# Optimization experiments

Measured on AMD Instinct MI355X. Metric: run time of the kernel, lower is better.

The kernel has to match this reference:

```python
import jax, jax.numpy as jnp
import numpy as np

NUM_HEADS = 6

def setup_inputs() -> dict:
    key = jax.random.key(0)
    ks = jax.random.split(key, 5)
    B, N, C = 4096, 49, 192
    nW = 64
    x = jax.random.normal(ks[0], (B, N, C), dtype=jnp.float32)
    mask = jax.random.normal(ks[1], (nW, 1, N, N), dtype=jnp.float32)
    w_qkv = jax.random.normal(ks[2], (C, 3 * C), dtype=jnp.float32) * (C ** -0.5)
    w_proj = jax.random.normal(ks[3], (C, C), dtype=jnp.float32) * (C ** -0.5)
    b_proj = jnp.zeros((C,), dtype=jnp.float32)
    return {"x": x, "mask": mask, "w_qkv": w_qkv, "w_proj": w_proj, "b_proj": b_proj}

def reference(x, mask, w_qkv, w_proj, b_proj):
    B, N, C = x.shape
    H = NUM_HEADS
    d = C // H
    nW = mask.shape[0]
    scale = d ** -0.5
    # fused QKV projection: [B, N, 3, H, d]
    qkv = (x @ w_qkv).reshape(B, N, 3, H, d)
    q = qkv[:, :, 0] * scale          # [B, N, H, d]
    k = qkv[:, :, 1]
    v = qkv[:, :, 2]
    # scaled attention scores per head: [B, H, N, N]
    attn = jnp.einsum('bnhd,bmhd->bhnm', q, k)
    # additive window mask, broadcast over heads
    attn = attn.reshape(B // nW, nW, H, N, N) + mask
    attn = attn.reshape(B, H, N, N)
    attn = jax.nn.softmax(attn, axis=-1)
    # attention-weighted values, back to [B, N, C]
    out = jnp.einsum('bhnm,bmhd->bnhd', attn, v).reshape(B, N, C)
    return out @ w_proj + b_proj
```

## Files before the change

### kernel.cpp

```cpp
#include <hip/hip_runtime.h>

using bf16_t = __bf16;
using bf16x4 = __bf16 __attribute__((ext_vector_type(4)));
using bf16x8 = __bf16 __attribute__((ext_vector_type(8)));
using f32x4  = float  __attribute__((ext_vector_type(4)));

#define MFMA16(a, b, c) __builtin_amdgcn_mfma_f32_16x16x32_bf16((a), (b), (c), 0, 0, 0)

__device__ __forceinline__ bf16x8 ld_b8_2x(const bf16_t* p) {
    bf16x4 lo = *(const bf16x4*)p;
    bf16x4 hi = *(const bf16x4*)(p + 4);
    bf16x8 r;
    r[0] = lo[0]; r[1] = lo[1]; r[2] = lo[2]; r[3] = lo[3];
    r[4] = hi[0]; r[5] = hi[1]; r[6] = hi[2]; r[7] = hi[3];
    return r;
}

__global__ void prep_weights(const float* __restrict__ wqkv,
                             const float* __restrict__ wproj,
                             bf16_t* __restrict__ wA,
                             bf16_t* __restrict__ w2B) {
    int idx = blockIdx.x * 256 + threadIdx.x;
    const int N1 = 36 * 6 * 64 * 8;
    if (idx < N1) {
        int j = idx & 7, L = (idx >> 3) & 63, q = idx >> 9;
        int ks = q % 6, mt = q / 6;
        int cc = ks * 32 + (L >> 4) * 8 + j;
        int ch = mt * 16 + (L & 15);
        wA[idx] = (bf16_t)wqkv[cc * 576 + ch];
    } else {
        int idx2 = idx - N1;
        if (idx2 < 6 * 12 * 64 * 8) {
            int j = idx2 & 7, L = (idx2 >> 3) & 63, q = idx2 >> 9;
            int nt = q % 12, ks = q / 12;
            int cc = ks * 32 + (L >> 4) * 8 + j;
            int ch = nt * 16 + (L & 15);
            w2B[idx2] = (bf16_t)wproj[cc * 192 + ch];
        }
    }
}

__global__ __launch_bounds__(1024, 4) void fused_window_attn(
    const float* __restrict__ x,
    const float* __restrict__ mask,
    const bf16_t* __restrict__ wA,
    const bf16_t* __restrict__ w2B,
    const float* __restrict__ bias,
    float* __restrict__ out)
{
    constexpr int QP  = 40;
    constexpr int VP  = 36;
    constexpr int PMP = 72;
    constexpr int AOP = 204;

    __shared__ __align__(16) char smem[147456];
    bf16_t* qS  = (bf16_t*)smem;
    bf16_t* kS  = qS + 15360;
    bf16_t* vS  = qS + 30720;
    bf16_t* pmS = qS + 44544;
    char*   pB  = smem + 98304;
    bf16_t* xS  = (bf16_t*)(smem + 98304);
    bf16_t* aoS = (bf16_t*)smem;

    const int b    = blockIdx.x;
    const int tid  = threadIdx.x;
    const int wid  = tid >> 6;
    const int lane = tid & 63;
    const int g    = lane >> 4;
    const int c    = lane & 15;

    const float* xb = x + (size_t)b * (49 * 192);
    for (int ch4 = tid; ch4 < 64 * 48; ch4 += 1024) {
        int tok = ch4 / 48, c4 = ch4 % 48;
        f32x4 v = (f32x4){0.f, 0.f, 0.f, 0.f};
        if (tok < 49) v = *(const f32x4*)(xb + tok * 192 + c4 * 4);
        bf16x4 o = {(bf16_t)v[0], (bf16_t)v[1], (bf16_t)v[2], (bf16_t)v[3]};
        *(bf16x4*)(xS + tok * AOP + c4 * 4) = o;
    }
    const float* mw = mask + (size_t)(b & 63) * (49 * 49);
    for (int idx = tid; idx < 64 * 64; idx += 1024) {
        int i = idx >> 6, t = idx & 63;
        float v;
        if (t < 49) v = (i < 49) ? mw[i * 49 + t] : 0.0f;
        else        v = -1e30f;
        pmS[i * PMP + t] = (bf16_t)v;
    }
    __syncthreads();

    const int nmt = (wid < 4) ? 3 : 2;
    const int mt0 = (wid < 4) ? wid * 3 : 12 + (wid - 4) * 2;

    f32x4 acc[3][4];
#pragma unroll
    for (int m = 0; m < 3; ++m)
#pragma unroll
        for (int n = 0; n < 4; ++n) acc[m][n] = (f32x4){0.f, 0.f, 0.f, 0.f};

#pragma unroll
    for (int ks = 0; ks < 6; ++ks) {
        bf16x8 Bf[4];
#pragma unroll
        for (int nt = 0; nt < 4; ++nt)
            Bf[nt] = ld_b8_2x(xS + (nt * 16 + c) * AOP + ks * 32 + g * 8);
#pragma unroll
        for (int m = 0; m < 3; ++m) {
            if (m < nmt) {
                int mt = mt0 + m;
                bf16x8 Af = *(const bf16x8*)(wA + (((size_t)mt * 6 + ks) * 64 + lane) * 8);
#pragma unroll
                for (int nt = 0; nt < 4; ++nt)
                    acc[m][nt] = MFMA16(Af, Bf[nt], acc[m][nt]);
            }
        }
    }

#pragma unroll
    for (int m = 0; m < 3; ++m) {
        if (m < nmt) {
            int mt  = mt0 + m;
            int typ = mt / 12;
            int rel = (mt - typ * 12) * 16 + g * 4;
            int hh  = rel >> 5;
            int dd0 = rel & 31;
#pragma unroll
            for (int nt = 0; nt < 4; ++nt) {
                int tok = nt * 16 + c;
                f32x4 a = acc[m][nt];
                bf16x4 v4 = {(bf16_t)a[0], (bf16_t)a[1], (bf16_t)a[2], (bf16_t)a[3]};
                if (typ == 0)      *(bf16x4*)(qS + hh * (64 * QP) + tok * QP + dd0) = v4;
                else if (typ == 1) *(bf16x4*)(kS + hh * (64 * QP) + tok * QP + dd0) = v4;
                else               *(bf16x4*)(vS + hh * (64 * VP) + tok * VP + dd0) = v4;
            }
        }
    }
    __syncthreads();

    const int h = wid >> 1;
    const int u = wid & 1;
    f32x4 oacc[2][2];
#pragma unroll
    for (int a0 = 0; a0 < 2; ++a0)
#pragma unroll
        for (int a1 = 0; a1 < 2; ++a1) oacc[a0][a1] = (f32x4){0.f, 0.f, 0.f, 0.f};

    if (wid < 12) {
        const bf16_t* qh = qS + h * (64 * QP);
        const bf16_t* kh = kS + h * (64 * QP);
        const bf16_t* vh = vS + h * (64 * VP);
        char*         Ph = pB + h * 8192;

        bf16x8 Ak[4], Bq[2];
#pragma unroll
        for (int mt = 0; mt < 4; ++mt)
            Ak[mt] = *(const bf16x8*)(kh + (mt * 16 + c) * QP + g * 8);
#pragma unroll
        for (int nl = 0; nl < 2; ++nl)
            Bq[nl] = *(const bf16x8*)(qh + ((2 * u + nl) * 16 + c) * QP + g * 8);

        f32x4 sacc[4][2];
#pragma unroll
        for (int mt = 0; mt < 4; ++mt)
#pragma unroll
            for (int nl = 0; nl < 2; ++nl) sacc[mt][nl] = (f32x4){0.f, 0.f, 0.f, 0.f};
#pragma unroll
        for (int mt = 0; mt < 4; ++mt)
#pragma unroll
            for (int nl = 0; nl < 2; ++nl)
                sacc[mt][nl] = MFMA16(Ak[mt], Bq[nl], sacc[mt][nl]);

        const float scale = 0.17677669529663687f;
#pragma unroll
        for (int nl = 0; nl < 2; ++nl) {
            int i = (2 * u + nl) * 16 + c;
            float s[16];
            float mx = -3.0e38f;
#pragma unroll
            for (int mt = 0; mt < 4; ++mt) {
                bf16x4 pmv = *(const bf16x4*)(pmS + i * PMP + mt * 16 + g * 4);
#pragma unroll
                for (int r = 0; r < 4; ++r) {
                    float sv = sacc[mt][nl][r] * scale + (float)pmv[r];
                    s[mt * 4 + r] = sv;
                    mx = fmaxf(mx, sv);
                }
            }
            mx = fmaxf(mx, __shfl_xor(mx, 16));
            mx = fmaxf(mx, __shfl_xor(mx, 32));
            float sum = 0.f;
#pragma unroll
            for (int k2 = 0; k2 < 16; ++k2) {
                float p = __expf(s[k2] - mx);
                s[k2] = p;
                sum += p;
            }
            sum += __shfl_xor(sum, 16);
            sum += __shfl_xor(sum, 32);
            float linv = 1.0f / sum;
#pragma unroll
            for (int mt = 0; mt < 4; ++mt) {
                int tc = 2 * mt + (g >> 1);
                bf16x4 p4 = {(bf16_t)(s[mt * 4 + 0] * linv), (bf16_t)(s[mt * 4 + 1] * linv),
                             (bf16_t)(s[mt * 4 + 2] * linv), (bf16_t)(s[mt * 4 + 3] * linv)};
                *(bf16x4*)(Ph + i * 128 + ((tc ^ (i & 7)) << 4) + ((g & 1) << 3)) = p4;
            }
        }

#pragma unroll
        for (int ks = 0; ks < 2; ++ks) {
            bf16x8 Bv[2];
#pragma unroll
            for (int nd = 0; nd < 2; ++nd) {
                bf16x8 t;
#pragma unroll
                for (int j = 0; j < 8; ++j)
                    t[j] = vh[(ks * 32 + g * 8 + j) * VP + nd * 16 + c];
                Bv[nd] = t;
            }
#pragma unroll
            for (int nl = 0; nl < 2; ++nl) {
                int i = (2 * u + nl) * 16 + c;
                bf16x8 Ap = *(const bf16x8*)(Ph + i * 128 + (((4 * ks + g) ^ (i & 7)) << 4));
#pragma unroll
                for (int nd = 0; nd < 2; ++nd)
                    oacc[nl][nd] = MFMA16(Ap, Bv[nd], oacc[nl][nd]);
            }
        }
    }
    __syncthreads();

    if (wid < 12) {
#pragma unroll
        for (int nl = 0; nl < 2; ++nl)
#pragma unroll
            for (int nd = 0; nd < 2; ++nd) {
                f32x4 o = oacc[nl][nd];
#pragma unroll
                for (int r = 0; r < 4; ++r) {
                    int i = (2 * u + nl) * 16 + 4 * g + r;
                    aoS[i * AOP + h * 32 + nd * 16 + c] = (bf16_t)o[r];
                }
            }
    }
    __syncthreads();

    const int mt = wid & 3;
    const int g3 = wid >> 2;
    f32x4 pacc[3];
#pragma unroll
    for (int j = 0; j < 3; ++j) pacc[j] = (f32x4){0.f, 0.f, 0.f, 0.f};

#pragma unroll
    for (int ks = 0; ks < 6; ++ks) {
        bf16x8 Ao = ld_b8_2x(aoS + (mt * 16 + c) * AOP + ks * 32 + g * 8);
#pragma unroll
        for (int j = 0; j < 3; ++j) {
            bf16x8 Bw = *(const bf16x8*)(w2B + (((size_t)ks * 12 + g3 * 3 + j) * 64 + lane) * 8);
            pacc[j] = MFMA16(Ao, Bw, pacc[j]);
        }
    }

    float* ob = out + (size_t)b * (49 * 192);
#pragma unroll
    for (int j = 0; j < 3; ++j) {
        int ch2 = (g3 * 3 + j) * 16 + c;
        float bbv = bias[ch2];
        f32x4 a = pacc[j];
#pragma unroll
        for (int r = 0; r < 4; ++r) {
            int tok = mt * 16 + 4 * g + r;
            if (tok < 49) ob[(size_t)tok * 192 + ch2] = a[r] + bbv;
        }
    }
}

extern "C" void kernel_launch(void* const* d_in, const int* in_sizes, int n_in,
                              void* d_out, int out_size, void* d_ws, size_t ws_size,
                              hipStream_t stream) {
    const float* x     = (const float*)d_in[0];
    const float* mask  = (const float*)d_in[1];
    const float* wqkv  = (const float*)d_in[2];
    const float* wproj = (const float*)d_in[3];
    const float* bias  = (const float*)d_in[4];
    float* out = (float*)d_out;

    bf16_t* wA  = (bf16_t*)d_ws;
    bf16_t* w2B = wA + 110592;

    prep_weights<<<576, 256, 0, stream>>>(wqkv, wproj, wA, w2B);
    fused_window_attn<<<4096, 1024, 0, stream>>>(x, mask, wA, w2B, bias, out);
}
```

Before: 415.3 us.

## Make attention kernel persistent over 16 windows with prefetched x and transposed V

The launch drops from 4096 blocks to 256 persistent blocks, each looping over 16 windows that share one mask slice (b & 63 is constant across the loop). The next window's x is loaded into registers during the current QKV GEMM and written to shared memory late, overlapping global loads with compute. The mask and bias are loaded once per block, and weight fragments are double-buffered. V is stored transposed so PV B-fragments become vector loads. The cost is one block per 256 CUs with 1024 threads, which leaves occupancy and latency hiding dependent on a single resident block per CU, plus extra barriers.

```diff
diff --git a/kernel.cpp b/kernel.cpp
--- a/kernel.cpp
+++ b/kernel.cpp
@@ -49,17 +49,17 @@
     float* __restrict__ out)
 {
     constexpr int QP  = 40;
-    constexpr int VP  = 36;
+    constexpr int VTP = 68;
     constexpr int PMP = 72;
     constexpr int AOP = 204;
 
-    __shared__ __align__(16) char smem[147456];
+    __shared__ __align__(16) char smem[145920];
     bf16_t* qS  = (bf16_t*)smem;
     bf16_t* kS  = qS + 15360;
-    bf16_t* vS  = qS + 30720;
-    bf16_t* pmS = qS + 44544;
-    char*   pB  = smem + 98304;
-    bf16_t* xS  = (bf16_t*)(smem + 98304);
+    bf16_t* vT  = qS + 30720;
+    bf16_t* pmS = qS + 43776;
+    char*   pB  = smem + 96768;
+    bf16_t* xS  = (bf16_t*)(smem + 96768);
     bf16_t* aoS = (bf16_t*)smem;
 
     const int b    = blockIdx.x;
@@ -69,15 +69,15 @@
     const int g    = lane >> 4;
     const int c    = lane & 15;
 
-    const float* xb = x + (size_t)b * (49 * 192);
-    for (int ch4 = tid; ch4 < 64 * 48; ch4 += 1024) {
-        int tok = ch4 / 48, c4 = ch4 % 48;
-        f32x4 v = (f32x4){0.f, 0.f, 0.f, 0.f};
-        if (tok < 49) v = *(const f32x4*)(xb + tok * 192 + c4 * 4);
-        bf16x4 o = {(bf16_t)v[0], (bf16_t)v[1], (bf16_t)v[2], (bf16_t)v[3]};
-        *(bf16x4*)(xS + tok * AOP + c4 * 4) = o;
-    }
-    const float* mw = mask + (size_t)(b & 63) * (49 * 49);
+    int tokA[3], cA[3];
+#pragma unroll
+    for (int i2 = 0; i2 < 3; ++i2) {
+        int ch4 = tid + 1024 * i2;
+        tokA[i2] = ch4 / 48;
+        cA[i2]   = ch4 % 48;
+    }
+
+    const float* mw = mask + (size_t)(b & 63) * 2401;
     for (int idx = tid; idx < 64 * 64; idx += 1024) {
         int i = idx >> 6, t = idx & 63;
         float v;
@@ -85,190 +85,261 @@
         else        v = -1e30f;
         pmS[i * PMP + t] = (bf16_t)v;
     }
+
+    f32x4 xr[3];
+    {
+        const float* xb = x + (size_t)b * 9408;
+#pragma unroll
+        for (int i2 = 0; i2 < 3; ++i2)
+            xr[i2] = (tokA[i2] < 49) ? *(const f32x4*)(xb + tokA[i2] * 192 + cA[i2] * 4)
+                                     : (f32x4){0.f, 0.f, 0.f, 0.f};
+    }
+#pragma unroll
+    for (int i2 = 0; i2 < 3; ++i2) {
+        f32x4 v = xr[i2];
+        bf16x4 o = {(bf16_t)v[0], (bf16_t)v[1], (bf16_t)v[2], (bf16_t)v[3]};
+        *(bf16x4*)(xS + tokA[i2] * AOP + cA[i2] * 4) = o;
+    }
     __syncthreads();
 
     const int nmt = (wid < 4) ? 3 : 2;
     const int mt0 = (wid < 4) ? wid * 3 : 12 + (wid - 4) * 2;
-
-    f32x4 acc[3][4];
-#pragma unroll
-    for (int m = 0; m < 3; ++m)
-#pragma unroll
-        for (int n = 0; n < 4; ++n) acc[m][n] = (f32x4){0.f, 0.f, 0.f, 0.f};
-
-#pragma unroll
-    for (int ks = 0; ks < 6; ++ks) {
-        bf16x8 Bf[4];
-#pragma unroll
-        for (int nt = 0; nt < 4; ++nt)
-            Bf[nt] = ld_b8_2x(xS + (nt * 16 + c) * AOP + ks * 32 + g * 8);
+    const int h   = wid >> 1;
+    const int u   = wid & 1;
+    const int mtc = wid & 3;
+    const int g3  = wid >> 2;
+
+    float bbv[3];
+#pragma unroll
+    for (int j = 0; j < 3; ++j) bbv[j] = bias[(g3 * 3 + j) * 16 + c];
+
+#pragma unroll 1
+    for (int it = 0; it < 16; ++it) {
+        f32x4 acc[3][4];
+#pragma unroll
+        for (int m = 0; m < 3; ++m)
+#pragma unroll
+            for (int n = 0; n < 4; ++n) acc[m][n] = (f32x4){0.f, 0.f, 0.f, 0.f};
+
+        bf16x8 Afc[3];
+#pragma unroll
+        for (int m = 0; m < 3; ++m)
+            if (m < nmt)
+                Afc[m] = *(const bf16x8*)(wA + (((size_t)(mt0 + m) * 6 + 0) * 64 + lane) * 8);
+
+#pragma unroll
+        for (int ks = 0; ks < 6; ++ks) {
+            bf16x8 Bf[4];
+#pragma unroll
+            for (int nt = 0; nt < 4; ++nt)
+                Bf[nt] = ld_b8_2x(xS + (nt * 16 + c) * AOP + ks * 32 + g * 8);
+            bf16x8 Afn[3];
+            if (ks < 5) {
+#pragma unroll
+                for (int m = 0; m < 3; ++m)
+                    if (m < nmt)
+                        Afn[m] = *(const bf16x8*)(wA + (((size_t)(mt0 + m) * 6 + ks + 1) * 64 + lane) * 8);
+            }
+#pragma unroll
+            for (int m = 0; m < 3; ++m) {
+                if (m < nmt) {
+#pragma unroll
+                    for (int nt = 0; nt < 4; ++nt)
+                        acc[m][nt] = MFMA16(Afc[m], Bf[nt], acc[m][nt]);
+                }
+            }
+            if (ks < 5) {
+#pragma unroll
+                for (int m = 0; m < 3; ++m) Afc[m] = Afn[m];
+            }
+        }
+
+        if (it < 15) {
+            const float* xb = x + (size_t)(b + 256 * (it + 1)) * 9408;
+#pragma unroll
+            for (int i2 = 0; i2 < 3; ++i2)
+                xr[i2] = (tokA[i2] < 49) ? *(const f32x4*)(xb + tokA[i2] * 192 + cA[i2] * 4)
+                                         : (f32x4){0.f, 0.f, 0.f, 0.f};
+        }
+
 #pragma unroll
         for (int m = 0; m < 3; ++m) {
             if (m < nmt) {
-                int mt = mt0 + m;
-                bf16x8 Af = *(const bf16x8*)(wA + (((size_t)mt * 6 + ks) * 64 + lane) * 8);
-#pragma unroll
-                for (int nt = 0; nt < 4; ++nt)
-                    acc[m][nt] = MFMA16(Af, Bf[nt], acc[m][nt]);
-            }
-        }
-    }
-
-#pragma unroll
-    for (int m = 0; m < 3; ++m) {
-        if (m < nmt) {
-            int mt  = mt0 + m;
-            int typ = mt / 12;
-            int rel = (mt - typ * 12) * 16 + g * 4;
-            int hh  = rel >> 5;
-            int dd0 = rel & 31;
-#pragma unroll
-            for (int nt = 0; nt < 4; ++nt) {
-                int tok = nt * 16 + c;
-                f32x4 a = acc[m][nt];
-                bf16x4 v4 = {(bf16_t)a[0], (bf16_t)a[1], (bf16_t)a[2], (bf16_t)a[3]};
-                if (typ == 0)      *(bf16x4*)(qS + hh * (64 * QP) + tok * QP + dd0) = v4;
-                else if (typ == 1) *(bf16x4*)(kS + hh * (64 * QP) + tok * QP + dd0) = v4;
-                else               *(bf16x4*)(vS + hh * (64 * VP) + tok * VP + dd0) = v4;
-            }
-        }
-    }
-    __syncthreads();
-
-    const int h = wid >> 1;
-    const int u = wid & 1;
-    f32x4 oacc[2][2];
-#pragma unroll
-    for (int a0 = 0; a0 < 2; ++a0)
-#pragma unroll
-        for (int a1 = 0; a1 < 2; ++a1) oacc[a0][a1] = (f32x4){0.f, 0.f, 0.f, 0.f};
-
-    if (wid < 12) {
-        const bf16_t* qh = qS + h * (64 * QP);
-        const bf16_t* kh = kS + h * (64 * QP);
-        const bf16_t* vh = vS + h * (64 * VP);
-        char*         Ph = pB + h * 8192;
+                int mt  = mt0 + m;
+                int typ = mt / 12;
+                int rel = (mt - typ * 12) * 16 + g * 4;
+                int hh  = rel >> 5;
+                int dd0 = rel & 31;
+#pragma unroll
+                for (int nt = 0; nt < 4; ++nt) {
+                    int tok = nt * 16 + c;
+                    f32x4 a = acc[m][nt];
+                    if (typ == 2) {
+#pragma unroll
+                        for (int r = 0; r < 4; ++r)
+                            vT[hh * 2176 + (dd0 + r) * VTP + tok] = (bf16_t)a[r];
+                    } else {
+                        bf16x4 v4 = {(bf16_t)a[0], (bf16_t)a[1], (bf16_t)a[2], (bf16_t)a[3]};
+                        if (typ == 0) *(bf16x4*)(qS + hh * 2560 + tok * QP + dd0) = v4;
+                        else          *(bf16x4*)(kS + hh * 2560 + tok * QP + dd0) = v4;
+                    }
+                }
+            }
+        }
+        __syncthreads();
 
         bf16x8 Ak[4], Bq[2];
-#pragma unroll
-        for (int mt = 0; mt < 4; ++mt)
-            Ak[mt] = *(const bf16x8*)(kh + (mt * 16 + c) * QP + g * 8);
-#pragma unroll
-        for (int nl = 0; nl < 2; ++nl)
-            Bq[nl] = *(const bf16x8*)(qh + ((2 * u + nl) * 16 + c) * QP + g * 8);
-
-        f32x4 sacc[4][2];
-#pragma unroll
-        for (int mt = 0; mt < 4; ++mt)
-#pragma unroll
-            for (int nl = 0; nl < 2; ++nl) sacc[mt][nl] = (f32x4){0.f, 0.f, 0.f, 0.f};
-#pragma unroll
-        for (int mt = 0; mt < 4; ++mt)
+        if (wid < 12) {
+            const bf16_t* qh = qS + h * 2560;
+            const bf16_t* kh = kS + h * 2560;
+#pragma unroll
+            for (int mt = 0; mt < 4; ++mt)
+                Ak[mt] = *(const bf16x8*)(kh + (mt * 16 + c) * QP + g * 8);
 #pragma unroll
             for (int nl = 0; nl < 2; ++nl)
-                sacc[mt][nl] = MFMA16(Ak[mt], Bq[nl], sacc[mt][nl]);
-
-        const float scale = 0.17677669529663687f;
-#pragma unroll
-        for (int nl = 0; nl < 2; ++nl) {
-            int i = (2 * u + nl) * 16 + c;
-            float s[16];
-            float mx = -3.0e38f;
-#pragma unroll
-            for (int mt = 0; mt < 4; ++mt) {
-                bf16x4 pmv = *(const bf16x4*)(pmS + i * PMP + mt * 16 + g * 4);
-#pragma unroll
-                for (int r = 0; r < 4; ++r) {
-                    float sv = sacc[mt][nl][r] * scale + (float)pmv[r];
-                    s[mt * 4 + r] = sv;
-                    mx = fmaxf(mx, sv);
-                }
-            }
-            mx = fmaxf(mx, __shfl_xor(mx, 16));
-            mx = fmaxf(mx, __shfl_xor(mx, 32));
-            float sum = 0.f;
-#pragma unroll
-            for (int k2 = 0; k2 < 16; ++k2) {
-                float p = __expf(s[k2] - mx);
-                s[k2] = p;
-                sum += p;
-            }
-            sum += __shfl_xor(sum, 16);
-            sum += __shfl_xor(sum, 32);
-            float linv = 1.0f / sum;
-#pragma unroll
-            for (int mt = 0; mt < 4; ++mt) {
-                int tc = 2 * mt + (g >> 1);
-                bf16x4 p4 = {(bf16_t)(s[mt * 4 + 0] * linv), (bf16_t)(s[mt * 4 + 1] * linv),
-                             (bf16_t)(s[mt * 4 + 2] * linv), (bf16_t)(s[mt * 4 + 3] * linv)};
-                *(bf16x4*)(Ph + i * 128 + ((tc ^ (i & 7)) << 4) + ((g & 1) << 3)) = p4;
-            }
-        }
-
-#pragma unroll
-        for (int ks = 0; ks < 2; ++ks) {
-            bf16x8 Bv[2];
-#pragma unroll
-            for (int nd = 0; nd < 2; ++nd) {
-                bf16x8 t;
-#pragma unroll
-                for (int j = 0; j < 8; ++j)
-                    t[j] = vh[(ks * 32 + g * 8 + j) * VP + nd * 16 + c];
-                Bv[nd] = t;
-            }
+                Bq[nl] = *(const bf16x8*)(qh + ((2 * u + nl) * 16 + c) * QP + g * 8);
+        }
+        __syncthreads();
+
+        f32x4 oacc[2][2];
+#pragma unroll
+        for (int a0 = 0; a0 < 2; ++a0)
+#pragma unroll
+            for (int a1 = 0; a1 < 2; ++a1) oacc[a0][a1] = (f32x4){0.f, 0.f, 0.f, 0.f};
+
+        if (wid < 12) {
+            char*         Ph = pB + h * 8192;
+            const bf16_t* vh = vT + h * 2176;
+
+            f32x4 sacc[4][2];
+#pragma unroll
+            for (int mt = 0; mt < 4; ++mt)
+#pragma unroll
+                for (int nl = 0; nl < 2; ++nl) sacc[mt][nl] = (f32x4){0.f, 0.f, 0.f, 0.f};
+#pragma unroll
+            for (int mt = 0; mt < 4; ++mt)
+#pragma unroll
+                for (int nl = 0; nl < 2; ++nl)
+                    sacc[mt][nl] = MFMA16(Ak[mt], Bq[nl], sacc[mt][nl]);
+
+            const float scale = 0.17677669529663687f;
 #pragma unroll
             for (int nl = 0; nl < 2; ++nl) {
                 int i = (2 * u + nl) * 16 + c;
-                bf16x8 Ap = *(const bf16x8*)(Ph + i * 128 + (((4 * ks + g) ^ (i & 7)) << 4));
+                float s[16];
+#pragma unroll
+                for (int mt = 0; mt < 4; ++mt) {
+                    bf16x4 pmv = *(const bf16x4*)(pmS + i * PMP + mt * 16 + g * 4);
+#pragma unroll
+                    for (int r = 0; r < 4; ++r)
+                        s[mt * 4 + r] = sacc[mt][nl][r] * scale + (float)pmv[r];
+                }
+                float m0 = fmaxf(fmaxf(fmaxf(s[0], s[1]), fmaxf(s[2], s[3])),
+                                 fmaxf(fmaxf(s[4], s[5]), fmaxf(s[6], s[7])));
+                float m1 = fmaxf(fmaxf(fmaxf(s[8], s[9]), fmaxf(s[10], s[11])),
+                                 fmaxf(fmaxf(s[12], s[13]), fmaxf(s[14], s[15])));
+                float mx = fmaxf(m0, m1);
+                mx = fmaxf(mx, __shfl_xor(mx, 16));
+                mx = fmaxf(mx, __shfl_xor(mx, 32));
+#pragma unroll
+                for (int k2 = 0; k2 < 16; ++k2) s[k2] = __expf(s[k2] - mx);
+                float s01 = (s[0] + s[1]) + (s[2] + s[3]);
+                float s23 = (s[4] + s[5]) + (s[6] + s[7]);
+                float s45 = (s[8] + s[9]) + (s[10] + s[11]);
+                float s67 = (s[12] + s[13]) + (s[14] + s[15]);
+                float sum = (s01 + s23) + (s45 + s67);
+                sum += __shfl_xor(sum, 16);
+                sum += __shfl_xor(sum, 32);
+                float linv = 1.0f / sum;
+#pragma unroll
+                for (int mt = 0; mt < 4; ++mt) {
+                    int tc = 2 * mt + (g >> 1);
+                    bf16x4 p4 = {(bf16_t)(s[mt * 4 + 0] * linv), (bf16_t)(s[mt * 4 + 1] * linv),
+                                 (bf16_t)(s[mt * 4 + 2] * linv), (bf16_t)(s[mt * 4 + 3] * linv)};
+                    *(bf16x4*)(Ph + i * 128 + ((tc ^ (i & 7)) << 4) + ((g & 1) << 3)) = p4;
+                }
+            }
+
+#pragma unroll
+            for (int ks = 0; ks < 2; ++ks) {
+                bf16x8 Bv[2];
 #pragma unroll
                 for (int nd = 0; nd < 2; ++nd)
-                    oacc[nl][nd] = MFMA16(Ap, Bv[nd], oacc[nl][nd]);
-            }
-        }
-    }
-    __syncthreads();
-
-    if (wid < 12) {
-#pragma unroll
-        for (int nl = 0; nl < 2; ++nl)
-#pragma unroll
-            for (int nd = 0; nd < 2; ++nd) {
-                f32x4 o = oacc[nl][nd];
-#pragma unroll
-                for (int r = 0; r < 4; ++r) {
-                    int i = (2 * u + nl) * 16 + 4 * g + r;
-                    aoS[i * AOP + h * 32 + nd * 16 + c] = (bf16_t)o[r];
-                }
-            }
-    }
-    __syncthreads();
-
-    const int mt = wid & 3;
-    const int g3 = wid >> 2;
-    f32x4 pacc[3];
-#pragma unroll
-    for (int j = 0; j < 3; ++j) pacc[j] = (f32x4){0.f, 0.f, 0.f, 0.f};
-
-#pragma unroll
-    for (int ks = 0; ks < 6; ++ks) {
-        bf16x8 Ao = ld_b8_2x(aoS + (mt * 16 + c) * AOP + ks * 32 + g * 8);
+                    Bv[nd] = ld_b8_2x(vh + (nd * 16 + c) * VTP + ks * 32 + g * 8);
+#pragma unroll
+                for (int nl = 0; nl < 2; ++nl) {
+                    int i = (2 * u + nl) * 16 + c;
+                    bf16x8 Ap = *(const bf16x8*)(Ph + i * 128 + (((4 * ks + g) ^ (i & 7)) << 4));
+#pragma unroll
+                    for (int nd = 0; nd < 2; ++nd)
+                        oacc[nl][nd] = MFMA16(Ap, Bv[nd], oacc[nl][nd]);
+                }
+            }
+
+#pragma unroll
+            for (int nl = 0; nl < 2; ++nl)
+#pragma unroll
+                for (int nd = 0; nd < 2; ++nd) {
+                    f32x4 o = oacc[nl][nd];
+#pragma unroll
+                    for (int r = 0; r < 4; ++r) {
+                        int i = (2 * u + nl) * 16 + 4 * g + r;
+                        aoS[i * AOP + h * 32 + nd * 16 + c] = (bf16_t)o[r];
+                    }
+                }
+        }
+        __syncthreads();
+
+        if (it < 15) {
+#pragma unroll
+            for (int i2 = 0; i2 < 3; ++i2) {
+                f32x4 v = xr[i2];
+                bf16x4 o = {(bf16_t)v[0], (bf16_t)v[1], (bf16_t)v[2], (bf16_t)v[3]};
+                *(bf16x4*)(xS + tokA[i2] * AOP + cA[i2] * 4) = o;
+            }
+        }
+
+        bf16x8 Ao[6];
+#pragma unroll
+        for (int ks = 0; ks < 6; ++ks)
+            Ao[ks] = ld_b8_2x(aoS + (mtc * 16 + c) * AOP + ks * 32 + g * 8);
+        __syncthreads();
+
+        f32x4 pacc[3];
+#pragma unroll
+        for (int j = 0; j < 3; ++j) pacc[j] = (f32x4){0.f, 0.f, 0.f, 0.f};
+
+        bf16x8 Bwc[3];
+#pragma unroll
+        for (int j = 0; j < 3; ++j)
+            Bwc[j] = *(const bf16x8*)(w2B + (((size_t)(g3 * 3 + j)) * 64 + lane) * 8);
+#pragma unroll
+        for (int ks = 0; ks < 6; ++ks) {
+            bf16x8 Bwn[3];
+            if (ks < 5) {
+#pragma unroll
+                for (int j = 0; j < 3; ++j)
+                    Bwn[j] = *(const bf16x8*)(w2B + (((size_t)(ks + 1) * 12 + g3 * 3 + j) * 64 + lane) * 8);
+            }
+#pragma unroll
+            for (int j = 0; j < 3; ++j)
+                pacc[j] = MFMA16(Ao[ks], Bwc[j], pacc[j]);
+            if (ks < 5) {
+#pragma unroll
+                for (int j = 0; j < 3; ++j) Bwc[j] = Bwn[j];
+            }
+        }
+
+        float* ob = out + (size_t)(b + 256 * it) * 9408;
 #pragma unroll
         for (int j = 0; j < 3; ++j) {
-            bf16x8 Bw = *(const bf16x8*)(w2B + (((size_t)ks * 12 + g3 * 3 + j) * 64 + lane) * 8);
-            pacc[j] = MFMA16(Ao, Bw, pacc[j]);
-        }
-    }
-
-    float* ob = out + (size_t)b * (49 * 192);
-#pragma unroll
-    for (int j = 0; j < 3; ++j) {
-        int ch2 = (g3 * 3 + j) * 16 + c;
-        float bbv = bias[ch2];
-        f32x4 a = pacc[j];
-#pragma unroll
-        for (int r = 0; r < 4; ++r) {
-            int tok = mt * 16 + 4 * g + r;
-            if (tok < 49) ob[(size_t)tok * 192 + ch2] = a[r] + bbv;
+            int ch2 = (g3 * 3 + j) * 16 + c;
+            f32x4 a2 = pacc[j];
+#pragma unroll
+            for (int r = 0; r < 4; ++r) {
+                int tok = mtc * 16 + 4 * g + r;
+                if (tok < 49) ob[(size_t)tok * 192 + ch2] = a2[r] + bbv[j];
+            }
         }
     }
 }
@@ -287,5 +358,5 @@
     bf16_t* w2B = wA + 110592;
 
     prep_weights<<<576, 256, 0, stream>>>(wqkv, wproj, wA, w2B);
-    fused_window_attn<<<4096, 1024, 0, stream>>>(x, mask, wA, w2B, bias, out);
+    fused_window_attn<<<256, 1024, 0, stream>>>(x, mask, wA, w2B, bias, out);
 }
```

New measurement: 870.8 us. 110% more time.

## Store V transposed, load Q/K fragments before a barrier, drop a barrier

Applied to the files above, without the earlier changes.

V is now written to shared memory transposed (d-major, token-contiguous), so the PV MFMA B-fragments load with two vector reads instead of eight scalar strided loads. Q/K fragments are read into registers before an added barrier. That frees the later phase to overwrite shared memory holding the attention output, which removes the barrier between PV and the aoS store. Softmax max and sum use tree reductions, and the bias load is hoisted to the kernel start. The V write becomes scattered scalar stores, which may add bank conflicts.

```diff
diff --git a/kernel.cpp b/kernel.cpp
--- a/kernel.cpp
+++ b/kernel.cpp
@@ -49,17 +49,17 @@
     float* __restrict__ out)
 {
     constexpr int QP  = 40;
-    constexpr int VP  = 36;
+    constexpr int VTP = 68;
     constexpr int PMP = 72;
     constexpr int AOP = 204;
 
-    __shared__ __align__(16) char smem[147456];
+    __shared__ __align__(16) char smem[145920];
     bf16_t* qS  = (bf16_t*)smem;
     bf16_t* kS  = qS + 15360;
-    bf16_t* vS  = qS + 30720;
-    bf16_t* pmS = qS + 44544;
-    char*   pB  = smem + 98304;
-    bf16_t* xS  = (bf16_t*)(smem + 98304);
+    bf16_t* vT  = qS + 30720;
+    bf16_t* pmS = qS + 43776;
+    char*   pB  = smem + 96768;
+    bf16_t* xS  = (bf16_t*)(smem + 96768);
     bf16_t* aoS = (bf16_t*)smem;
 
     const int b    = blockIdx.x;
@@ -68,6 +68,12 @@
     const int lane = tid & 63;
     const int g    = lane >> 4;
     const int c    = lane & 15;
+
+    const int mtc = wid & 3;
+    const int g3  = wid >> 2;
+    float bbv[3];
+#pragma unroll
+    for (int j = 0; j < 3; ++j) bbv[j] = bias[(g3 * 3 + j) * 16 + c];
 
     const float* xb = x + (size_t)b * (49 * 192);
     for (int ch4 = tid; ch4 < 64 * 48; ch4 += 1024) {
@@ -126,10 +132,15 @@
             for (int nt = 0; nt < 4; ++nt) {
                 int tok = nt * 16 + c;
                 f32x4 a = acc[m][nt];
-                bf16x4 v4 = {(bf16_t)a[0], (bf16_t)a[1], (bf16_t)a[2], (bf16_t)a[3]};
-                if (typ == 0)      *(bf16x4*)(qS + hh * (64 * QP) + tok * QP + dd0) = v4;
-                else if (typ == 1) *(bf16x4*)(kS + hh * (64 * QP) + tok * QP + dd0) = v4;
-                else               *(bf16x4*)(vS + hh * (64 * VP) + tok * VP + dd0) = v4;
+                if (typ == 2) {
+#pragma unroll
+                    for (int r = 0; r < 4; ++r)
+                        vT[hh * (32 * VTP) + (dd0 + r) * VTP + tok] = (bf16_t)a[r];
+                } else {
+                    bf16x4 v4 = {(bf16_t)a[0], (bf16_t)a[1], (bf16_t)a[2], (bf16_t)a[3]};
+                    if (typ == 0) *(bf16x4*)(qS + hh * (64 * QP) + tok * QP + dd0) = v4;
+                    else          *(bf16x4*)(kS + hh * (64 * QP) + tok * QP + dd0) = v4;
+                }
             }
         }
     }
@@ -137,25 +148,23 @@
 
     const int h = wid >> 1;
     const int u = wid & 1;
-    f32x4 oacc[2][2];
-#pragma unroll
-    for (int a0 = 0; a0 < 2; ++a0)
-#pragma unroll
-        for (int a1 = 0; a1 < 2; ++a1) oacc[a0][a1] = (f32x4){0.f, 0.f, 0.f, 0.f};
-
+
+    bf16x8 Ak[4], Bq[2];
     if (wid < 12) {
         const bf16_t* qh = qS + h * (64 * QP);
         const bf16_t* kh = kS + h * (64 * QP);
-        const bf16_t* vh = vS + h * (64 * VP);
-        char*         Ph = pB + h * 8192;
-
-        bf16x8 Ak[4], Bq[2];
 #pragma unroll
         for (int mt = 0; mt < 4; ++mt)
             Ak[mt] = *(const bf16x8*)(kh + (mt * 16 + c) * QP + g * 8);
 #pragma unroll
         for (int nl = 0; nl < 2; ++nl)
             Bq[nl] = *(const bf16x8*)(qh + ((2 * u + nl) * 16 + c) * QP + g * 8);
+    }
+    __syncthreads();
+
+    if (wid < 12) {
+        char*         Ph = pB + h * 8192;
+        const bf16_t* vh = vT + h * (32 * VTP);
 
         f32x4 sacc[4][2];
 #pragma unroll
@@ -173,26 +182,26 @@
         for (int nl = 0; nl < 2; ++nl) {
             int i = (2 * u + nl) * 16 + c;
             float s[16];
-            float mx = -3.0e38f;
 #pragma unroll
             for (int mt = 0; mt < 4; ++mt) {
                 bf16x4 pmv = *(const bf16x4*)(pmS + i * PMP + mt * 16 + g * 4);
 #pragma unroll
-                for (int r = 0; r < 4; ++r) {
-                    float sv = sacc[mt][nl][r] * scale + (float)pmv[r];
-                    s[mt * 4 + r] = sv;
-                    mx = fmaxf(mx, sv);
-                }
-            }
+                for (int r = 0; r < 4; ++r)
+                    s[mt * 4 + r] = sacc[mt][nl][r] * scale + (float)pmv[r];
+            }
+            float mx = fmaxf(
+                fmaxf(fmaxf(fmaxf(s[0], s[1]), s[2]), fmaxf(fmaxf(s[3], s[4]), s[5])),
+                fmaxf(fmaxf(fmaxf(s[6], s[7]), s[8]), fmaxf(fmaxf(s[9], s[10]), s[11])));
+            mx = fmaxf(mx, fmaxf(fmaxf(s[12], s[13]), fmaxf(s[14], s[15])));
             mx = fmaxf(mx, __shfl_xor(mx, 16));
             mx = fmaxf(mx, __shfl_xor(mx, 32));
-            float sum = 0.f;
-#pragma unroll
-            for (int k2 = 0; k2 < 16; ++k2) {
-                float p = __expf(s[k2] - mx);
-                s[k2] = p;
-                sum += p;
-            }
+#pragma unroll
+            for (int k2 = 0; k2 < 16; ++k2) s[k2] = __expf(s[k2] - mx);
+            float s01 = (s[0] + s[1]) + (s[2] + s[3]);
+            float s23 = (s[4] + s[5]) + (s[6] + s[7]);
+            float s45 = (s[8] + s[9]) + (s[10] + s[11]);
+            float s67 = (s[12] + s[13]) + (s[14] + s[15]);
+            float sum = (s01 + s23) + (s45 + s67);
             sum += __shfl_xor(sum, 16);
             sum += __shfl_xor(sum, 32);
             float linv = 1.0f / sum;
@@ -205,17 +214,18 @@
             }
         }
 
+        f32x4 oacc[2][2];
+#pragma unroll
+        for (int a0 = 0; a0 < 2; ++a0)
+#pragma unroll
+            for (int a1 = 0; a1 < 2; ++a1) oacc[a0][a1] = (f32x4){0.f, 0.f, 0.f, 0.f};
+
 #pragma unroll
         for (int ks = 0; ks < 2; ++ks) {
             bf16x8 Bv[2];
 #pragma unroll
-            for (int nd = 0; nd < 2; ++nd) {
-                bf16x8 t;
-#pragma unroll
-                for (int j = 0; j < 8; ++j)
-                    t[j] = vh[(ks * 32 + g * 8 + j) * VP + nd * 16 + c];
-                Bv[nd] = t;
-            }
+            for (int nd = 0; nd < 2; ++nd)
+                Bv[nd] = ld_b8_2x(vh + (nd * 16 + c) * VTP + ks * 32 + g * 8);
 #pragma unroll
             for (int nl = 0; nl < 2; ++nl) {
                 int i = (2 * u + nl) * 16 + c;
@@ -225,10 +235,7 @@
                     oacc[nl][nd] = MFMA16(Ap, Bv[nd], oacc[nl][nd]);
             }
         }
-    }
-    __syncthreads();
-
-    if (wid < 12) {
+
 #pragma unroll
         for (int nl = 0; nl < 2; ++nl)
 #pragma unroll
@@ -243,15 +250,13 @@
     }
     __syncthreads();
 
-    const int mt = wid & 3;
-    const int g3 = wid >> 2;
     f32x4 pacc[3];
 #pragma unroll
     for (int j = 0; j < 3; ++j) pacc[j] = (f32x4){0.f, 0.f, 0.f, 0.f};
 
 #pragma unroll
     for (int ks = 0; ks < 6; ++ks) {
-        bf16x8 Ao = ld_b8_2x(aoS + (mt * 16 + c) * AOP + ks * 32 + g * 8);
+        bf16x8 Ao = ld_b8_2x(aoS + (mtc * 16 + c) * AOP + ks * 32 + g * 8);
 #pragma unroll
         for (int j = 0; j < 3; ++j) {
             bf16x8 Bw = *(const bf16x8*)(w2B + (((size_t)ks * 12 + g3 * 3 + j) * 64 + lane) * 8);
@@ -263,12 +268,11 @@
 #pragma unroll
     for (int j = 0; j < 3; ++j) {
         int ch2 = (g3 * 3 + j) * 16 + c;
-        float bbv = bias[ch2];
         f32x4 a = pacc[j];
 #pragma unroll
         for (int r = 0; r < 4; ++r) {
-            int tok = mt * 16 + 4 * g + r;
-            if (tok < 49) ob[(size_t)tok * 192 + ch2] = a[r] + bbv;
+            int tok = mtc * 16 + 4 * g + r;
+            if (tok < 49) ob[(size_t)tok * 192 + ch2] = a[r] + bbv[j];
         }
     }
 }
```

Measured after the change: 408.7 us. About the same (-1.6%).
